# Kernel optimization log

Measured on AMD Instinct MI355X. Metric: run time of the kernel, lower is better.

## Reference

```python
import jax, jax.numpy as jnp
import numpy as np

NMS_THRESH = 0.5
SCORE_THRESH = 0.2
MAX_SUBJECT = 15
MAX_OBJECT = 15
B, NS, NO = 32, 512, 512


def _make_boxes(k, b, n):
    u = jax.random.uniform(k, (b, n, 4))
    xy = u[..., :2] * 1000.0          # top-left corner
    wh = u[..., 2:] * 200.0 + 1.0     # positive width/height
    return jnp.concatenate([xy, xy + wh], axis=-1)  # valid xyxy boxes


def setup_inputs() -> dict:
    key = jax.random.key(0)
    ks = jax.random.split(key, 6)
    return {
        "subj_boxes": _make_boxes(ks[0], B, NS),
        "subj_scores": jax.random.uniform(ks[1], (B, NS)),
        "subj_labels": jax.random.randint(ks[2], (B, NS), 0, 30, dtype=jnp.int32),
        "obj_boxes": _make_boxes(ks[3], B, NO),
        "obj_scores": jax.random.uniform(ks[4], (B, NO)),
        "obj_labels": jax.random.randint(ks[5], (B, NO), 0, 30, dtype=jnp.int32),
    }


def reference(subj_boxes, subj_scores, subj_labels, obj_boxes, obj_scores, obj_labels):
    # concat subject + object detections per image, as in preprocess()
    boxes = jnp.concatenate([subj_boxes, obj_boxes], axis=1)    # [B,N,4]
    scores = jnp.concatenate([subj_scores, obj_scores], axis=1) # [B,N]
    labels = jnp.concatenate([subj_labels, obj_labels], axis=1) # [B,N]
    b, n = scores.shape
    is_subj = jnp.arange(n) < subj_boxes.shape[1]               # [N]

    # sort by score descending (matches the argsort after NMS; greedy NMS
    # preserves this ordering among survivors)
    order = jnp.argsort(-scores, axis=1)
    boxes = jnp.take_along_axis(boxes, order[..., None], axis=1)
    scores = jnp.take_along_axis(scores, order, axis=1)
    labels = jnp.take_along_axis(labels, order, axis=1)
    is_subj = jnp.take(is_subj, order)                          # [B,N]

    active = scores >= SCORE_THRESH

    # torchvision batched_nms: offset boxes per class so distinct classes
    # never overlap (comparisons only -> no gradient path)
    max_coord = jax.lax.stop_gradient(jnp.max(boxes))
    ob = boxes + labels.astype(boxes.dtype)[..., None] * (max_coord + 1.0)

    # pairwise IoU [B,N,N]
    area = (ob[..., 2] - ob[..., 0]) * (ob[..., 3] - ob[..., 1])
    lt = jnp.maximum(ob[:, :, None, :2], ob[:, None, :, :2])
    rb = jnp.minimum(ob[:, :, None, 2:], ob[:, None, :, 2:])
    wh = jnp.clip(rb - lt, 0.0)
    inter = wh[..., 0] * wh[..., 1]
    iou = inter / (area[:, :, None] + area[:, None, :] - inter)

    later = jnp.arange(n)[None, :] > jnp.arange(n)[:, None]     # strictly lower-score

    def body(i, suppressed):  # greedy NMS, vectorized over batch
        keep_i = active[:, i] & ~suppressed[:, i]
        return suppressed | (keep_i[:, None] & (iou[:, i, :] > NMS_THRESH) & later[i])

    suppressed = jax.lax.fori_loop(0, n, body, jnp.zeros((b, n), dtype=bool))
    kept = active & ~suppressed

    # split survivors into subjects / objects, keep top max_subject/max_object
    neg = jnp.finfo(scores.dtype).min
    sub_key = jnp.where(kept & is_subj, scores, neg)
    obj_key = jnp.where(kept & ~is_subj, scores, neg)
    sv, si = jax.lax.top_k(sub_key, MAX_SUBJECT)
    ov, oi = jax.lax.top_k(obj_key, MAX_OBJECT)
    idx = jnp.concatenate([si, oi], axis=1)                     # [B,K]
    valid = jnp.concatenate([sv, ov], axis=1) > neg             # [B,K]

    out_boxes = jnp.take_along_axis(boxes, idx[..., None], axis=1) * valid[..., None]
    out_scores = jnp.take_along_axis(scores, idx, axis=1) * valid
    out_labels = jnp.where(valid, jnp.take_along_axis(labels, idx, axis=1), -1)
    num_subjects = jnp.sum(sv > neg, axis=1)
    return out_boxes, out_scores, out_labels, num_subjects, valid
```

## Files before the change

### kernel.cpp

```cpp
#include <hip/hip_runtime.h>
#include <stdint.h>

#define BQ    32
#define NSUB  512
#define NDET  1024
#define NCLS  30
#define KSLOT 30
#define BCAP  96

#pragma clang fp contract(off)

typedef unsigned long long u64;

__global__ __launch_bounds__(512) void bucket_kernel(
    const float* __restrict__ sb, const float* __restrict__ ss,
    const int*   __restrict__ sl,
    const float* __restrict__ ob, const float* __restrict__ os,
    const int*   __restrict__ ol,
    float* __restrict__ pmax, int* __restrict__ cnts,
    u64* __restrict__ bkeys, float4* __restrict__ bboxes)
{
    const int b = blockIdx.x, t = threadIdx.x;
    const int lane = t & 63, w = t >> 6;
    __shared__ int   lcnt[NCLS];
    __shared__ float wred[8];

    if (t < NCLS) lcnt[t] = 0;

    float4 bxs = *(const float4*)(sb + (size_t)(b * NSUB + t) * 4);
    float4 bxo = *(const float4*)(ob + (size_t)(b * NSUB + t) * 4);
    float scs = ss[b * NSUB + t];  int lbs = sl[b * NSUB + t];
    float sco = os[b * NSUB + t];  int lbo = ol[b * NSUB + t];

    float m = fmaxf(fmaxf(fmaxf(bxs.x, bxs.y), fmaxf(bxs.z, bxs.w)),
                    fmaxf(fmaxf(bxo.x, bxo.y), fmaxf(bxo.z, bxo.w)));
    for (int off = 32; off; off >>= 1) m = fmaxf(m, __shfl_xor(m, off));
    if (lane == 0) wred[w] = m;
    __syncthreads();
    if (t == 0) {
        float mm = wred[0];
        for (int i = 1; i < 8; ++i) mm = fmaxf(mm, wred[i]);
        pmax[b] = mm;
    }

    if (scs >= 0.2f) {
        int pos = atomicAdd(&lcnt[lbs], 1);
        if (pos < BCAP) {
            size_t s = ((size_t)b * NCLS + lbs) * BCAP + pos;
            bkeys[s]  = ((u64)__float_as_uint(scs) << 32) | (u64)(1023 - t);
            bboxes[s] = bxs;
        }
    }
    if (sco >= 0.2f) {
        int pos = atomicAdd(&lcnt[lbo], 1);
        if (pos < BCAP) {
            size_t s = ((size_t)b * NCLS + lbo) * BCAP + pos;
            bkeys[s]  = ((u64)__float_as_uint(sco) << 32) | (u64)(1023 - (512 + t));
            bboxes[s] = bxo;
        }
    }
    __syncthreads();
    if (t < NCLS) {
        int c = lcnt[t];
        cnts[b * NCLS + t] = (c < BCAP) ? c : BCAP;
    }
}

__global__ __launch_bounds__(64) void nms_class_kernel(
    const float* __restrict__ pmax, const int* __restrict__ cnts,
    const u64* __restrict__ bkeys, const float4* __restrict__ bboxes,
    u64* __restrict__ subk, u64* __restrict__ objk,
    float4* __restrict__ subb, float4* __restrict__ objb)
{
#pragma clang fp contract(off)
    const int c    = blockIdx.x;
    const int b    = blockIdx.y;
    const int lane = threadIdx.x;

    __shared__ u64    keyarr[BCAP];
    __shared__ u64    skey[BCAP];
    __shared__ float4 bxs4[BCAP];

    const size_t base = (size_t)b * NCLS + c;

    u64    K1 = bkeys[base * BCAP + lane];
    float4 B1 = bboxes[base * BCAP + lane];
    u64 K2 = 0; float4 B2 = make_float4(0.f, 0.f, 0.f, 0.f);
    if (lane < BCAP - 64) {
        K2 = bkeys[base * BCAP + 64 + lane];
        B2 = bboxes[base * BCAP + 64 + lane];
    }
    const int cnt = cnts[base];
    float pv = pmax[lane & 31];
    for (int off = 32; off; off >>= 1) pv = fmaxf(pv, __shfl_xor(pv, off));
    const float mco  = pv + 1.0f;
    const float offc = (float)c * mco;

    keyarr[lane] = K1;
    if (lane < BCAP - 64) keyarr[64 + lane] = K2;
    __threadfence_block();

    {
        int r = 0;
        for (int l = 0; l < cnt; ++l) r += (keyarr[l] > K1) ? 1 : 0;
        if (lane < cnt) { skey[r] = K1; bxs4[r] = B1; }
    }
    if (cnt > 64) {
        int e = 64 + lane;
        int r = 0;
        for (int l = 0; l < cnt; ++l) r += (keyarr[l] > K2) ? 1 : 0;
        if (e < cnt) { skey[r] = K2; bxs4[r] = B2; }
    }
    __threadfence_block();

    const int  lim1  = (cnt < 64) ? cnt : 64;
    const bool have1 = (lane < lim1);
    u64 SK1 = have1 ? skey[lane] : 0;
    int idx1 = 1023 - (int)(unsigned)(SK1 & 0xffffffffull);
    float4 bj1 = have1 ? bxs4[lane] : make_float4(0.f, 0.f, 0.f, 0.f);
    const bool have2 = (64 + lane) < cnt;
    u64 SK2 = 0; int idx2 = 0; float4 bj2 = make_float4(0.f, 0.f, 0.f, 0.f);
    if (cnt > 64) {
        SK2 = have2 ? skey[64 + lane] : 0;
        idx2 = 1023 - (int)(unsigned)(SK2 & 0xffffffffull);
        if (have2) bj2 = bxs4[64 + lane];
    }

    float j0 = bj1.x + offc, j1 = bj1.y + offc;
    float j2v = bj1.z + offc, j3 = bj1.w + offc;
    float aj = (j2v - j0) * (j3 - j1);
    u64 ov = 0;
    for (int l = 0; l < lim1; ++l) {
        float4 bl = bxs4[l];
        float i0 = bl.x + offc, i1 = bl.y + offc;
        float i2 = bl.z + offc, i3 = bl.w + offc;
        float ai = (i2 - i0) * (i3 - i1);
        if (have1 && l < lane) {
            float ltx = fmaxf(i0, j0), lty = fmaxf(i1, j1);
            float rbx = fminf(i2, j2v), rby = fminf(i3, j3);
            float wx = fmaxf(rbx - ltx, 0.0f), wy = fmaxf(rby - lty, 0.0f);
            float inter = wx * wy;
            float iou = inter / ((ai + aj) - inter);
            if (iou > 0.5f) ov |= (1ull << l);
        }
    }
    u64 keptm = 0;
    {
        u64 undec = __ballot(have1);
        while (undec) {
            int l = (int)__ffsll((unsigned long long)undec) - 1;
            keptm |= (1ull << l);
            u64 supby = __ballot(((ov >> l) & 1ull) != 0ull);
            undec &= ~(supby | (1ull << l));
        }
    }
    const bool kept1 = have1 && ((keptm >> lane) & 1ull);
    const u64 keptA = __ballot(kept1);

    bool kept2 = false;
    if (cnt > 64) {
        float k0 = bj2.x + offc, k1 = bj2.y + offc;
        float k2 = bj2.z + offc, k3 = bj2.w + offc;
        float ak = (k2 - k0) * (k3 - k1);
        bool sup2 = !have2;
        u64 ka = keptA;
        while (ka) {
            int l = (int)__ffsll((unsigned long long)ka) - 1;
            ka &= ka - 1ull;
            float4 bl = bxs4[l];
            float i0 = bl.x + offc, i1 = bl.y + offc;
            float i2 = bl.z + offc, i3 = bl.w + offc;
            float ai = (i2 - i0) * (i3 - i1);
            if (!sup2) {
                float ltx = fmaxf(i0, k0), lty = fmaxf(i1, k1);
                float rbx = fminf(i2, k2), rby = fminf(i3, k3);
                float wx = fmaxf(rbx - ltx, 0.0f), wy = fmaxf(rby - lty, 0.0f);
                float inter = wx * wy;
                float iou = inter / ((ai + ak) - inter);
                if (iou > 0.5f) sup2 = true;
            }
        }
        u64 ov2 = 0;
        const int lim2 = cnt - 64;
        for (int l = 0; l < lim2; ++l) {
            float4 bl = bxs4[64 + l];
            float i0 = bl.x + offc, i1 = bl.y + offc;
            float i2 = bl.z + offc, i3 = bl.w + offc;
            float ai = (i2 - i0) * (i3 - i1);
            if (have2 && l < lane) {
                float ltx = fmaxf(i0, k0), lty = fmaxf(i1, k1);
                float rbx = fminf(i2, k2), rby = fminf(i3, k3);
                float wx = fmaxf(rbx - ltx, 0.0f), wy = fmaxf(rby - lty, 0.0f);
                float inter = wx * wy;
                float iou = inter / ((ai + ak) - inter);
                if (iou > 0.5f) ov2 |= (1ull << l);
            }
        }
        u64 keptm2 = 0;
        u64 undec2 = __ballot(have2 && !sup2);
        while (undec2) {
            int l = (int)__ffsll((unsigned long long)undec2) - 1;
            keptm2 |= (1ull << l);
            u64 supby = __ballot(((ov2 >> l) & 1ull) != 0ull);
            undec2 &= ~(supby | (1ull << l));
        }
        kept2 = have2 && !sup2 && ((keptm2 >> lane) & 1ull);
    }

    const bool s1 = kept1 && (idx1 < NSUB), o1 = kept1 && (idx1 >= NSUB);
    const bool s2 = kept2 && (idx2 < NSUB), o2 = kept2 && (idx2 >= NSUB);
    const u64 mS1 = __ballot(s1), mS2 = __ballot(s2);
    const u64 mO1 = __ballot(o1), mO2 = __ballot(o2);
    const u64 ltm = (1ull << lane) - 1ull;
    u64*    subp = subk + base * 15;   float4* sbbp = subb + base * 15;
    u64*    objp = objk + base * 15;   float4* obbp = objb + base * 15;
    if (s1) { int p = (int)__popcll(mS1 & ltm); if (p < 15) { subp[p] = SK1; sbbp[p] = bj1; } }
    if (s2) { int p = (int)__popcll(mS1) + (int)__popcll(mS2 & ltm); if (p < 15) { subp[p] = SK2; sbbp[p] = bj2; } }
    if (o1) { int p = (int)__popcll(mO1 & ltm); if (p < 15) { objp[p] = SK1; obbp[p] = bj1; } }
    if (o2) { int p = (int)__popcll(mO1) + (int)__popcll(mO2 & ltm); if (p < 15) { objp[p] = SK2; obbp[p] = bj2; } }
    int tS = (int)(__popcll(mS1) + __popcll(mS2)); if (tS > 15) tS = 15;
    int tO = (int)(__popcll(mO1) + __popcll(mO2)); if (tO > 15) tO = 15;
    if (lane >= tS && lane < 15) subp[lane] = 0;
    if (lane >= tO && lane < 15) objp[lane] = 0;
}

__global__ __launch_bounds__(512) void select_kernel(
    const u64* __restrict__ subk, const u64* __restrict__ objk,
    const float4* __restrict__ subb, const float4* __restrict__ objb,
    float* __restrict__ out)
{
    const int b    = blockIdx.x;
    const int side = blockIdx.y;
    const int t    = threadIdx.x;
    const int N    = NCLS * 15;

    float* outB = out;
    float* outS = out + BQ * KSLOT * 4;
    float* outL = outS + BQ * KSLOT;
    float* outN = outL + BQ * KSLOT;
    float* outV = outN + BQ;

    const u64*    src  = (side ? objk : subk) + (size_t)b * N;
    const float4* srcb = (side ? objb : subb) + (size_t)b * N;

    __shared__ u64 ckey[N + 64];
    __shared__ int cntv;

    if (t == 0) cntv = 0;
    __syncthreads();

    u64 k = (t < N) ? src[t] : 0;
    int pos = -1;
    if (k != 0) pos = atomicAdd(&cntv, 1);
    if (pos >= 0) ckey[pos] = k;
    __syncthreads();
    const int nv  = cntv;
    const int nvc = (nv < 15) ? nv : 15;

    if (pos >= 0) {
        int rank = 0;
        for (int l = 0; l < nv; ++l) rank += (ckey[l] > k) ? 1 : 0;
        if (rank < 15) {
            int p = b * KSLOT + (side ? (15 + rank) : rank);
            float4 bx = srcb[t];
            *(float4*)(outB + (size_t)p * 4) = bx;
            outS[p] = __uint_as_float((unsigned)(k >> 32));
            outL[p] = (float)(t / 15);
            outV[p] = 1.0f;
        }
    }
    if (t >= nvc && t < 15) {
        int p = b * KSLOT + (side ? (15 + t) : t);
        *(float4*)(outB + (size_t)p * 4) = make_float4(0.f, 0.f, 0.f, 0.f);
        outS[p] = 0.0f; outL[p] = -1.0f; outV[p] = 0.0f;
    }
    if (side == 0 && t == 0) outN[b] = (float)nvc;
}

extern "C" void kernel_launch(void* const* d_in, const int* in_sizes, int n_in,
                              void* d_out, int out_size, void* d_ws, size_t ws_size,
                              hipStream_t stream) {
    const float* sb = (const float*)d_in[0];
    const float* ss = (const float*)d_in[1];
    const int*   sl = (const int*)d_in[2];
    const float* ob = (const float*)d_in[3];
    const float* os = (const float*)d_in[4];
    const int*   ol = (const int*)d_in[5];

    float*  pmax   = (float*)d_ws;
    int*    cnts   = (int*)((char*)d_ws + 256);
    u64*    bkeys  = (u64*)((char*)d_ws + 8192);
    float4* bboxes = (float4*)((char*)d_ws + 745472);
    u64*    subk   = (u64*)((char*)d_ws + 2220032);
    u64*    objk   = subk + (size_t)BQ * NCLS * 15;
    float4* subb   = (float4*)((char*)d_ws + 2450432);
    float4* objb   = subb + (size_t)BQ * NCLS * 15;

    bucket_kernel<<<dim3(BQ), dim3(512), 0, stream>>>(
        sb, ss, sl, ob, os, ol, pmax, cnts, bkeys, bboxes);
    nms_class_kernel<<<dim3(NCLS, BQ), dim3(64), 0, stream>>>(
        pmax, cnts, bkeys, bboxes, subk, objk, subb, objb);
    select_kernel<<<dim3(BQ, 2), dim3(512), 0, stream>>>(
        subk, objk, subb, objb, (float*)d_out);
}
```

Measured before the change: 82.28 us.

## Fuse class bucketing into per-class NMS kernel via ballot compaction

The first kernel is reduced to only the per-image max-coordinate reduction. Each per-class NMS block now scans all 1024 scores and labels of its image, compacts the matching detections with ballot/popcount into shared memory, and gathers their boxes straight from the inputs. This drops the global bucket key/box arrays, the shared atomics, and one round-trip through workspace memory. In exchange every class block re-reads the full score and label arrays (30x redundant reads per image) and does scattered box gathers, and the bucket order changes from atomic order to index order.

```diff
diff --git a/kernel.cpp b/kernel.cpp
--- a/kernel.cpp
+++ b/kernel.cpp
@@ -12,28 +12,19 @@
 
 typedef unsigned long long u64;
 
-__global__ __launch_bounds__(512) void bucket_kernel(
-    const float* __restrict__ sb, const float* __restrict__ ss,
-    const int*   __restrict__ sl,
-    const float* __restrict__ ob, const float* __restrict__ os,
-    const int*   __restrict__ ol,
-    float* __restrict__ pmax, int* __restrict__ cnts,
-    u64* __restrict__ bkeys, float4* __restrict__ bboxes)
+__global__ __launch_bounds__(512) void pmax_kernel(
+    const float* __restrict__ sb, const float* __restrict__ ob,
+    float* __restrict__ pmax)
 {
     const int b = blockIdx.x, t = threadIdx.x;
     const int lane = t & 63, w = t >> 6;
-    __shared__ int   lcnt[NCLS];
     __shared__ float wred[8];
-
-    if (t < NCLS) lcnt[t] = 0;
-
-    float4 bxs = *(const float4*)(sb + (size_t)(b * NSUB + t) * 4);
-    float4 bxo = *(const float4*)(ob + (size_t)(b * NSUB + t) * 4);
-    float scs = ss[b * NSUB + t];  int lbs = sl[b * NSUB + t];
-    float sco = os[b * NSUB + t];  int lbo = ol[b * NSUB + t];
-
-    float m = fmaxf(fmaxf(fmaxf(bxs.x, bxs.y), fmaxf(bxs.z, bxs.w)),
-                    fmaxf(fmaxf(bxo.x, bxo.y), fmaxf(bxo.z, bxo.w)));
+    const float4* sb4 = (const float4*)sb;
+    const float4* ob4 = (const float4*)ob;
+    float4 a  = sb4[(size_t)b * NSUB + t];
+    float4 c4 = ob4[(size_t)b * NSUB + t];
+    float m = fmaxf(fmaxf(fmaxf(a.x, a.y), fmaxf(a.z, a.w)),
+                    fmaxf(fmaxf(c4.x, c4.y), fmaxf(c4.z, c4.w)));
     for (int off = 32; off; off >>= 1) m = fmaxf(m, __shfl_xor(m, off));
     if (lane == 0) wred[w] = m;
     __syncthreads();
@@ -42,33 +33,14 @@
         for (int i = 1; i < 8; ++i) mm = fmaxf(mm, wred[i]);
         pmax[b] = mm;
     }
-
-    if (scs >= 0.2f) {
-        int pos = atomicAdd(&lcnt[lbs], 1);
-        if (pos < BCAP) {
-            size_t s = ((size_t)b * NCLS + lbs) * BCAP + pos;
-            bkeys[s]  = ((u64)__float_as_uint(scs) << 32) | (u64)(1023 - t);
-            bboxes[s] = bxs;
-        }
-    }
-    if (sco >= 0.2f) {
-        int pos = atomicAdd(&lcnt[lbo], 1);
-        if (pos < BCAP) {
-            size_t s = ((size_t)b * NCLS + lbo) * BCAP + pos;
-            bkeys[s]  = ((u64)__float_as_uint(sco) << 32) | (u64)(1023 - (512 + t));
-            bboxes[s] = bxo;
-        }
-    }
-    __syncthreads();
-    if (t < NCLS) {
-        int c = lcnt[t];
-        cnts[b * NCLS + t] = (c < BCAP) ? c : BCAP;
-    }
 }
 
 __global__ __launch_bounds__(64) void nms_class_kernel(
-    const float* __restrict__ pmax, const int* __restrict__ cnts,
-    const u64* __restrict__ bkeys, const float4* __restrict__ bboxes,
+    const float* __restrict__ sb, const float* __restrict__ ss,
+    const int*   __restrict__ sl,
+    const float* __restrict__ ob, const float* __restrict__ os,
+    const int*   __restrict__ ol,
+    const float* __restrict__ pmax,
     u64* __restrict__ subk, u64* __restrict__ objk,
     float4* __restrict__ subb, float4* __restrict__ objb)
 {
@@ -77,39 +49,75 @@
     const int b    = blockIdx.y;
     const int lane = threadIdx.x;
 
-    __shared__ u64    keyarr[BCAP];
+    __shared__ u64    ukey[BCAP];
     __shared__ u64    skey[BCAP];
     __shared__ float4 bxs4[BCAP];
 
-    const size_t base = (size_t)b * NCLS + c;
-
-    u64    K1 = bkeys[base * BCAP + lane];
-    float4 B1 = bboxes[base * BCAP + lane];
-    u64 K2 = 0; float4 B2 = make_float4(0.f, 0.f, 0.f, 0.f);
-    if (lane < BCAP - 64) {
-        K2 = bkeys[base * BCAP + 64 + lane];
-        B2 = bboxes[base * BCAP + 64 + lane];
-    }
-    const int cnt = cnts[base];
+    const float4* sb4 = (const float4*)sb;
+    const float4* ob4 = (const float4*)ob;
+
+    float rsc[16]; int rlb[16];
+    #pragma unroll
+    for (int it = 0; it < 16; ++it) {
+        int i = it * 64 + lane;
+        if (it < 8) {
+            rsc[it] = ss[b * NSUB + i];
+            rlb[it] = sl[b * NSUB + i];
+        } else {
+            rsc[it] = os[b * NSUB + i - NSUB];
+            rlb[it] = ol[b * NSUB + i - NSUB];
+        }
+    }
+
     float pv = pmax[lane & 31];
     for (int off = 32; off; off >>= 1) pv = fmaxf(pv, __shfl_xor(pv, off));
     const float mco  = pv + 1.0f;
     const float offc = (float)c * mco;
 
-    keyarr[lane] = K1;
-    if (lane < BCAP - 64) keyarr[64 + lane] = K2;
+    ukey[lane] = 0;
+    if (lane < BCAP - 64) ukey[64 + lane] = 0;
     __threadfence_block();
+
+    int cbase = 0;
+    const u64 ltm0 = (1ull << lane) - 1ull;
+    #pragma unroll
+    for (int it = 0; it < 16; ++it) {
+        int i = it * 64 + lane;
+        bool match = (rsc[it] >= 0.2f) && (rlb[it] == c);
+        u64 bal = __ballot(match);
+        if (match) {
+            int pos = cbase + (int)__popcll(bal & ltm0);
+            if (pos < BCAP) {
+                ukey[pos] = ((u64)__float_as_uint(rsc[it]) << 32) | (u64)(1023 - i);
+            }
+        }
+        cbase += (int)__popcll(bal);
+    }
+    const int cnt = (cbase < BCAP) ? cbase : BCAP;
+    __threadfence_block();
+
+    u64 K1 = ukey[lane];
+    int gi1 = 1023 - (int)(unsigned)(K1 & 0xffffffffull);
+    float4 B1 = (gi1 < NSUB) ? sb4[(size_t)b * NSUB + gi1]
+                             : ob4[(size_t)b * NSUB + gi1 - NSUB];
+    u64 K2k = 0; float4 B2 = make_float4(0.f, 0.f, 0.f, 0.f);
+    if (cnt > 64 && lane < BCAP - 64) {
+        K2k = ukey[64 + lane];
+        int gi2 = 1023 - (int)(unsigned)(K2k & 0xffffffffull);
+        B2 = (gi2 < NSUB) ? sb4[(size_t)b * NSUB + gi2]
+                          : ob4[(size_t)b * NSUB + gi2 - NSUB];
+    }
 
     {
         int r = 0;
-        for (int l = 0; l < cnt; ++l) r += (keyarr[l] > K1) ? 1 : 0;
+        for (int l = 0; l < cnt; ++l) r += (ukey[l] > K1) ? 1 : 0;
         if (lane < cnt) { skey[r] = K1; bxs4[r] = B1; }
     }
     if (cnt > 64) {
         int e = 64 + lane;
         int r = 0;
-        for (int l = 0; l < cnt; ++l) r += (keyarr[l] > K2) ? 1 : 0;
-        if (e < cnt) { skey[r] = K2; bxs4[r] = B2; }
+        for (int l = 0; l < cnt; ++l) r += (ukey[l] > K2k) ? 1 : 0;
+        if (e < cnt) { skey[r] = K2k; bxs4[r] = B2; }
     }
     __threadfence_block();
 
@@ -207,6 +215,7 @@
         kept2 = have2 && !sup2 && ((keptm2 >> lane) & 1ull);
     }
 
+    const size_t base = (size_t)b * NCLS + c;
     const bool s1 = kept1 && (idx1 < NSUB), o1 = kept1 && (idx1 >= NSUB);
     const bool s2 = kept2 && (idx2 < NSUB), o2 = kept2 && (idx2 >= NSUB);
     const u64 mS1 = __ballot(s1), mS2 = __ballot(s2);
@@ -287,19 +296,15 @@
     const float* os = (const float*)d_in[4];
     const int*   ol = (const int*)d_in[5];
 
-    float*  pmax   = (float*)d_ws;
-    int*    cnts   = (int*)((char*)d_ws + 256);
-    u64*    bkeys  = (u64*)((char*)d_ws + 8192);
-    float4* bboxes = (float4*)((char*)d_ws + 745472);
-    u64*    subk   = (u64*)((char*)d_ws + 2220032);
-    u64*    objk   = subk + (size_t)BQ * NCLS * 15;
-    float4* subb   = (float4*)((char*)d_ws + 2450432);
-    float4* objb   = subb + (size_t)BQ * NCLS * 15;
-
-    bucket_kernel<<<dim3(BQ), dim3(512), 0, stream>>>(
-        sb, ss, sl, ob, os, ol, pmax, cnts, bkeys, bboxes);
+    float*  pmax = (float*)d_ws;
+    u64*    subk = (u64*)((char*)d_ws + 4096);
+    u64*    objk = (u64*)((char*)d_ws + 119296);
+    float4* subb = (float4*)((char*)d_ws + 234496);
+    float4* objb = (float4*)((char*)d_ws + 464896);
+
+    pmax_kernel<<<dim3(BQ), dim3(512), 0, stream>>>(sb, ob, pmax);
     nms_class_kernel<<<dim3(NCLS, BQ), dim3(64), 0, stream>>>(
-        pmax, cnts, bkeys, bboxes, subk, objk, subb, objb);
+        sb, ss, sl, ob, os, ol, pmax, subk, objk, subb, objb);
     select_kernel<<<dim3(BQ, 2), dim3(512), 0, stream>>>(
         subk, objk, subb, objb, (float*)d_out);
 }
```

Result: no change. 83.42 us (+1.4%).
